# Optimization experiments

Hardware: AMD Instinct MI355X
Metric: run time of the kernel (lower is better)

## Reference

```python
import jax, jax.numpy as jnp
import numpy as np

N, IN, H, OUT, C = 1024, 64, 64, 64, 32
EPS = 1e-5   # SAKELayer.epsilon
INF = 1e5    # SAKELayer.inf


def _w(key, i, o, scale=1.0):
    return jax.random.normal(key, (i, o), jnp.float32) * (scale / np.sqrt(i))


def setup_inputs() -> dict:
    key = jax.random.key(0)
    ks = jax.random.split(key, 16)
    return dict(
        h=jax.random.normal(ks[0], (N, IN), jnp.float32),
        x=jax.random.normal(ks[1], (N, 3), jnp.float32),
        # edge model (ConcatenationFilter): Linear(2*IN+1,H), SiLU, Linear(H,H)
        ew1=_w(ks[2], 2 * IN + 1, H), eb1=jnp.zeros((H,), jnp.float32),
        ew2=_w(ks[3], H, H), eb2=jnp.zeros((H,), jnp.float32),
        # node_mlp: Linear(2H+IN,H), SiLU, Linear(H,OUT)
        nw1=_w(ks[4], 2 * H + IN, H), nb1=jnp.zeros((H,), jnp.float32),
        nw2=_w(ks[5], H, OUT), nb2=jnp.zeros((OUT,), jnp.float32),
        # coordinate_mlp: Linear(H,H), SiLU, Linear(H,1,bias=False) xavier gain 1e-3
        cw1=_w(ks[6], H, H), cb1=jnp.zeros((H,), jnp.float32),
        cw2=_w(ks[7], H, 1, scale=1e-3),
        # semantic_attention_mlp: Linear(H,1), LeakyReLU
        aw=_w(ks[8], H, 1), ab=jnp.zeros((1,), jnp.float32),
        # coefficients_mlp: Linear(H,H), SiLU, Linear(H,C)
        fw1=_w(ks[9], H, H), fb1=jnp.zeros((H,), jnp.float32),
        fw2=_w(ks[10], H, C), fb2=jnp.zeros((C,), jnp.float32),
        # post_norm_mlp: Linear(C,H), SiLU, Linear(H,H)
        pw1=_w(ks[11], C, H), pb1=jnp.zeros((H,), jnp.float32),
        pw2=_w(ks[12], H, H), pb2=jnp.zeros((H,), jnp.float32),
        log_gamma=jnp.array(0.0, jnp.float32),
    )


def reference(h, x, ew1, eb1, ew2, eb2, nw1, nb1, nw2, nb2, cw1, cb1, cw2,
              aw, ab, fw1, fb1, fw2, fb2, pw1, pb1, pw2, pb2, log_gamma):
    n, d_in = h.shape
    silu = jax.nn.silu
    eye = jnp.eye(n, dtype=h.dtype)[:, :, None]                    # [n,n,1]

    x_minus_xt = x[:, None, :] - x[None, :, :]                     # [n,n,3]
    norm = jnp.sqrt(jnp.sum(x_minus_xt ** 2, -1, keepdims=True) + EPS)  # [n,n,1]

    h_cat_ht = jnp.concatenate(
        [jnp.broadcast_to(h[:, None, :], (n, n, d_in)),
         jnp.broadcast_to(h[None, :, :], (n, n, d_in))], -1)       # [n,n,2*IN]

    # edge model: MLP over concat(features, distance)
    e_in = jnp.concatenate([h_cat_ht, norm], -1)                   # [n,n,2*IN+1]
    h_e = silu(e_in @ ew1 + eb1) @ ew2 + eb2                       # [n,n,H]

    # euclidean attention over neighbors j (diag masked by +INF distance)
    att_e = jax.nn.softmax(-(norm + INF * eye) * jnp.exp(log_gamma), axis=1)
    # semantic attention
    att_s = jax.nn.softmax(jax.nn.leaky_relu(h_e @ aw + ab) - INF * eye, axis=1)
    comb = att_e * att_s
    comb = comb / (jnp.sum(comb, axis=1, keepdims=True) + EPS)     # [n,n,1]
    h_e_att = h_e * comb                                           # [n,n,H]

    # spatial attention: equivariant coefficient combinations
    coeff = silu(h_e_att @ fw1 + fb1) @ fw2 + fb2                  # [n,n,C]
    dirs = x_minus_xt / (norm + 1.0)                               # [n,n,3]
    combos = jnp.einsum('ijc,ijd->icd', coeff, dirs) / n           # mean over j -> [n,C,3]
    h_comb = silu(jnp.sum(combos ** 2, -1) @ pw1 + pb1) @ pw2 + pb2  # [n,H]

    # node update
    h_agg = jnp.sum(h_e_att, axis=1)                               # [n,H]
    node_in = jnp.concatenate([h, h_agg, h_comb], -1)              # [n,2H+IN]
    h_out = h + (silu(node_in @ nw1 + nb1) @ nw2 + nb2)            # residual

    # equivariant coordinate update
    phi = silu(h_e @ cw1 + cb1) @ cw2                              # [n,n,1]
    x_out = x + jnp.mean(x_minus_xt * phi, axis=1)                 # [n,3]
    return h_out, x_out
```

## Files before the change

### kernel.cpp

```cpp
#include <hip/hip_runtime.h>
#include <hip/hip_bf16.h>

#define NN 1024
#define JT 128
#define LSTR 72
#define EPSV 1e-5f
#define BIGINF 1e5f

typedef __attribute__((ext_vector_type(8))) short short8;
typedef __attribute__((ext_vector_type(4))) short short4v;
typedef __attribute__((ext_vector_type(4))) float f32x4;

__device__ __forceinline__ float siluf(float v) {
    return v * __builtin_amdgcn_rcpf(1.0f + __expf(-v));
}
__device__ __forceinline__ float pnorm(float dx, float dy, float dz) {
    return sqrtf(dx * dx + dy * dy + dz * dz + EPSV);
}
__device__ __forceinline__ float wsum(float v) {
#pragma unroll
    for (int off = 32; off > 0; off >>= 1) v += __shfl_xor(v, off, 64);
    return v;
}
__device__ __forceinline__ float red16(float v) {
    v += __shfl_xor(v, 1, 64); v += __shfl_xor(v, 2, 64);
    v += __shfl_xor(v, 4, 64); v += __shfl_xor(v, 8, 64);
    return v;
}
__device__ __forceinline__ float redquad(float v) {
    v += __shfl_xor(v, 16, 64); v += __shfl_xor(v, 32, 64);
    return v;
}
__device__ __forceinline__ short f2bs(float v) {
    __hip_bfloat16 b = __float2bfloat16(v);
    return *reinterpret_cast<short*>(&b);
}
__device__ __forceinline__ short f2bt(float v) {
    return (short)(__float_as_uint(v) >> 16);
}

__global__ void kA(const float* __restrict__ h, const float* __restrict__ ew1,
                   const float* __restrict__ eb1, const float* __restrict__ ew2,
                   const float* __restrict__ cw1, const float* __restrict__ fw1,
                   const float* __restrict__ fw2, const float* __restrict__ aw,
                   const float* __restrict__ ab, const float* __restrict__ eb2,
                   float* __restrict__ HA, float* __restrict__ HB,
                   float* __restrict__ HBT, short* __restrict__ ew2T,
                   short* __restrict__ cw1T, short* __restrict__ fw1T,
                   short* __restrict__ fw2T, float* __restrict__ wsv,
                   float* __restrict__ svb) {
    const int b = blockIdx.x;
    const int o = threadIdx.x;
    if (b < NN) {
        const int i = b;
        float hv = h[i * 64 + o];
        float a = 0.f, bb = eb1[o];
#pragma unroll
        for (int k = 0; k < 64; k++) {
            float hk = __shfl(hv, k, 64);
            a += hk * ew1[k * 64 + o];
            bb += hk * ew1[(64 + k) * 64 + o];
        }
        HA[i * 64 + o] = a;
        HB[i * 64 + o] = bb;
        HBT[o * NN + i] = bb;
    } else if (b < NN + 64) {
        const int r = b - NN;
        ew2T[r * 64 + o] = f2bs(ew2[o * 64 + r]);
        cw1T[r * 64 + o] = f2bs(cw1[o * 64 + r]);
        fw1T[r * 64 + o] = f2bs(fw1[o * 64 + r]);
        if (r < 32) fw2T[r * 64 + o] = f2bs(fw2[o * 32 + r]);
    } else {
        float s = 0.f;
#pragma unroll
        for (int q = 0; q < 64; q++) s += ew2[o * 64 + q] * aw[q];
        wsv[o] = s;
        float e = wsum(eb2[o] * aw[o]);
        if (o == 0) svb[0] = e + ab[0];
    }
}

__global__ __launch_bounds__(256) void kBn(
    const float* __restrict__ x, const float* __restrict__ ew1,
    const float* __restrict__ HA, const float* __restrict__ HBT,
    const float* __restrict__ wsv, const float* __restrict__ svb,
    const float* __restrict__ lg, float* __restrict__ ls,
    float* __restrict__ rowm, float* __restrict__ rowd) {
    const int i = blockIdx.x;
    const int t = threadIdx.x;
    const float* HAi = HA + i * 64;
    const float* w1 = ew1 + 128 * 64;
    const float gamma = __expf(lg[0]);
    const float svb0 = svb[0];
    const float xi0 = x[i * 3 + 0], xi1 = x[i * 3 + 1], xi2 = x[i * 3 + 2];

    float4 xa = ((const float4*)x)[3 * t + 0];
    float4 xb = ((const float4*)x)[3 * t + 1];
    float4 xc = ((const float4*)x)[3 * t + 2];
    float nrm[4], le[4], lv[4];
    {
        float dx0 = xi0 - xa.x, dy0 = xi1 - xa.y, dz0 = xi2 - xa.z;
        float dx1 = xi0 - xa.w, dy1 = xi1 - xb.x, dz1 = xi2 - xb.y;
        float dx2 = xi0 - xb.z, dy2 = xi1 - xb.w, dz2 = xi2 - xc.x;
        float dx3 = xi0 - xc.y, dy3 = xi1 - xc.z, dz3 = xi2 - xc.w;
        nrm[0] = pnorm(dx0, dy0, dz0);
        nrm[1] = pnorm(dx1, dy1, dz1);
        nrm[2] = pnorm(dx2, dy2, dz2);
        nrm[3] = pnorm(dx3, dy3, dz3);
    }
    float d0 = 0.f, d1 = 0.f, d2 = 0.f, d3 = 0.f;
#pragma unroll 8
    for (int k = 0; k < 64; k++) {
        float4 hb = *(const float4*)&HBT[k * NN + 4 * t];
        float hk = HAi[k], w1k = w1[k], wv = wsv[k];
        d0 += siluf(hk + hb.x + nrm[0] * w1k) * wv;
        d1 += siluf(hk + hb.y + nrm[1] * w1k) * wv;
        d2 += siluf(hk + hb.z + nrm[2] * w1k) * wv;
        d3 += siluf(hk + hb.w + nrm[3] * w1k) * wv;
    }
    float me = -3.0e38f, ms = -3.0e38f;
    float4 svo;
    {
        float dd[4] = {d0, d1, d2, d3};
#pragma unroll
        for (int m = 0; m < 4; m++) {
            int j = 4 * t + m;
            float sv = dd[m] + svb0;
            sv = sv >= 0.f ? sv : 0.01f * sv;
            if (j == i) sv -= BIGINF;
            lv[m] = sv;
            le[m] = -(nrm[m] + (j == i ? BIGINF : 0.f)) * gamma;
            me = fmaxf(me, le[m]);
            ms = fmaxf(ms, lv[m]);
        }
        svo.x = lv[0]; svo.y = lv[1]; svo.z = lv[2]; svo.w = lv[3];
    }
    *(float4*)&ls[(size_t)i * NN + 4 * t] = svo;

    __shared__ float sm[4], ss[4], s1[4], s2[4], s3[4];
#pragma unroll
    for (int off = 32; off > 0; off >>= 1) {
        me = fmaxf(me, __shfl_xor(me, off, 64));
        ms = fmaxf(ms, __shfl_xor(ms, off, 64));
    }
    const int w = t >> 6;
    if ((t & 63) == 0) { sm[w] = me; ss[w] = ms; }
    __syncthreads();
    me = fmaxf(fmaxf(sm[0], sm[1]), fmaxf(sm[2], sm[3]));
    ms = fmaxf(fmaxf(ss[0], ss[1]), fmaxf(ss[2], ss[3]));
    float Se = 0.f, Ss = 0.f, Sq = 0.f;
#pragma unroll
    for (int m = 0; m < 4; m++) {
        float ee = __expf(le[m] - me);
        float es = __expf(lv[m] - ms);
        Se += ee; Ss += es; Sq += ee * es;
    }
    Se = wsum(Se); Ss = wsum(Ss); Sq = wsum(Sq);
    if ((t & 63) == 0) { s1[w] = Se; s2[w] = Ss; s3[w] = Sq; }
    __syncthreads();
    if (t == 0) {
        rowm[i] = me + ms;
        rowd[i] = (s3[0] + s3[1] + s3[2] + s3[3]) +
                  EPSV * (s1[0] + s1[1] + s1[2] + s1[3]) * (s2[0] + s2[1] + s2[2] + s2[3]);
    }
}

__device__ __forceinline__ void stageW(const short* __restrict__ g, short* s,
                                       int tid, int rows) {
    for (int c = tid; c < rows * 16; c += 512) {
        int r = c >> 4, q = c & 15;
        *(short4v*)&s[r * LSTR + q * 4] = *(const short4v*)&g[r * 64 + q * 4];
    }
}

__global__ __launch_bounds__(512) void kD(
    const float* __restrict__ x, const float* __restrict__ ew1,
    const float* __restrict__ eb2, const float* __restrict__ cb1,
    const float* __restrict__ cw2, const float* __restrict__ fb1,
    const float* __restrict__ fb2, const float* __restrict__ lg,
    const float* __restrict__ HA, const float* __restrict__ HB,
    const short* __restrict__ ew2T, const short* __restrict__ cw1T,
    const short* __restrict__ fw1T, const short* __restrict__ fw2T,
    const float* __restrict__ ls, const float* __restrict__ rowm,
    const float* __restrict__ rowd, float* __restrict__ hagg,
    float* __restrict__ combos, float* __restrict__ xupd) {
    __shared__ __align__(16) short sHe[JT * LSTR];
    __shared__ __align__(16) short sW[64 * LSTR];
    __shared__ float sNrm[JT], sFx[JT], sFy[JT], sFz[JT];
    __shared__ float sDx[JT], sDy[JT], sDz[JT], sPh[JT];
    __shared__ float sComb[JT], sHag[64], sCombos[96];

    const int tid = threadIdx.x;
    const int i = blockIdx.x;
    const int jbase = blockIdx.y * JT;
    const int lane = tid & 63, w = tid >> 6;
    const int col = lane & 15, quad = lane >> 4;
    const int row = w * 16 + col;

    if (tid < JT) {
        int j = jbase + tid;
        float dx = x[i * 3 + 0] - x[j * 3 + 0];
        float dy = x[i * 3 + 1] - x[j * 3 + 1];
        float dz = x[i * 3 + 2] - x[j * 3 + 2];
        float nrm = pnorm(dx, dy, dz);
        float inv1 = __builtin_amdgcn_rcpf(nrm + 1.0f);
        sNrm[tid] = nrm;
        sDx[tid] = dx; sDy[tid] = dy; sDz[tid] = dz;
        sFx[tid] = dx * inv1; sFy[tid] = dy * inv1; sFz[tid] = dz * inv1;
        float gamma = __expf(lg[0]);
        float le = -(nrm + (j == i ? BIGINF : 0.f)) * gamma;
        sComb[tid] = __expf(le + ls[(size_t)i * NN + j] - rowm[i]) / rowd[i];
    } else if (tid < JT + 64) {
        sHag[tid - JT] = 0.f;
    } else if (tid < JT + 160) {
        sCombos[tid - JT - 64] = 0.f;
    }
    stageW(ew2T, sW, tid, 64);
    __syncthreads();

    f32x4 acc[4] = {{0.f, 0.f, 0.f, 0.f}, {0.f, 0.f, 0.f, 0.f},
                    {0.f, 0.f, 0.f, 0.f}, {0.f, 0.f, 0.f, 0.f}};
    {
        const int j = jbase + row;
        const float nrm = sNrm[row];
        short8 afr[2];
#pragma unroll
        for (int kb = 0; kb < 2; kb++) {
            const int k0 = kb * 32 + quad * 8;
            const float* hb = &HB[j * 64 + k0];
            const float* ha = &HA[i * 64 + k0];
            const float* w1 = &ew1[128 * 64 + k0];
#pragma unroll
            for (int t = 0; t < 8; t++)
                afr[kb][t] = f2bt(siluf(ha[t] + hb[t] + nrm * w1[t]));
        }
#pragma unroll
        for (int kb = 0; kb < 2; kb++) {
#pragma unroll
            for (int nb = 0; nb < 4; nb++) {
                short8 b = *(const short8*)&sW[(nb * 16 + col) * LSTR + kb * 32 + quad * 8];
                acc[nb] = __builtin_amdgcn_mfma_f32_16x16x32_bf16(afr[kb], b, acc[nb], 0, 0, 0);
            }
        }
    }
    {
        float eb[4];
#pragma unroll
        for (int nb = 0; nb < 4; nb++) eb[nb] = eb2[nb * 16 + col];
        float hv[4][4];
#pragma unroll
        for (int reg = 0; reg < 4; reg++) {
            int r = w * 16 + quad * 4 + reg;
#pragma unroll
            for (int nb = 0; nb < 4; nb++) {
                hv[nb][reg] = acc[nb][reg] + eb[nb];
                sHe[r * LSTR + nb * 16 + col] = f2bt(hv[nb][reg]);
            }
        }
#pragma unroll
        for (int nb = 0; nb < 4; nb++) {
            float v = 0.f;
#pragma unroll
            for (int reg = 0; reg < 4; reg++)
                v += hv[nb][reg] * sComb[w * 16 + quad * 4 + reg];
            v = redquad(v);
            if (quad == 0) atomicAdd(&sHag[nb * 16 + col], v);
        }
    }
    __syncthreads();
    stageW(cw1T, sW, tid, 64);
    __syncthreads();

    {
        f32x4 p[4] = {{0.f, 0.f, 0.f, 0.f}, {0.f, 0.f, 0.f, 0.f},
                      {0.f, 0.f, 0.f, 0.f}, {0.f, 0.f, 0.f, 0.f}};
        const short* ap = &sHe[row * LSTR + quad * 8];
#pragma unroll
        for (int kb = 0; kb < 2; kb++) {
            short8 a = *(const short8*)&ap[kb * 32];
#pragma unroll
            for (int nb = 0; nb < 4; nb++) {
                short8 b = *(const short8*)&sW[(nb * 16 + col) * LSTR + kb * 32 + quad * 8];
                p[nb] = __builtin_amdgcn_mfma_f32_16x16x32_bf16(a, b, p[nb], 0, 0, 0);
            }
        }
        float cbv[4], cwv[4];
#pragma unroll
        for (int nb = 0; nb < 4; nb++) { cbv[nb] = cb1[nb * 16 + col]; cwv[nb] = cw2[nb * 16 + col]; }
#pragma unroll
        for (int reg = 0; reg < 4; reg++) {
            float ph = 0.f;
#pragma unroll
            for (int nb = 0; nb < 4; nb++) ph += siluf(p[nb][reg] + cbv[nb]) * cwv[nb];
            ph = red16(ph);
            if (col == 0) sPh[w * 16 + quad * 4 + reg] = ph;
        }
    }
    __syncthreads();
    stageW(fw1T, sW, tid, 64);
    __syncthreads();

    f32x4 vacc[4] = {{0.f, 0.f, 0.f, 0.f}, {0.f, 0.f, 0.f, 0.f},
                     {0.f, 0.f, 0.f, 0.f}, {0.f, 0.f, 0.f, 0.f}};
    {
        const short* ap = &sHe[row * LSTR + quad * 8];
#pragma unroll
        for (int kb = 0; kb < 2; kb++) {
            short8 a = *(const short8*)&ap[kb * 32];
#pragma unroll
            for (int nb = 0; nb < 4; nb++) {
                short8 b = *(const short8*)&sW[(nb * 16 + col) * LSTR + kb * 32 + quad * 8];
                vacc[nb] = __builtin_amdgcn_mfma_f32_16x16x32_bf16(a, b, vacc[nb], 0, 0, 0);
            }
        }
    }
    short wvs[4][4];
    {
        float fbv[4];
#pragma unroll
        for (int nb = 0; nb < 4; nb++) fbv[nb] = fb1[nb * 16 + col];
#pragma unroll
        for (int reg = 0; reg < 4; reg++) {
            float cm = sComb[w * 16 + quad * 4 + reg];
#pragma unroll
            for (int nb = 0; nb < 4; nb++)
                wvs[reg][nb] = f2bt(siluf(cm * vacc[nb][reg] + fbv[nb]));
        }
    }
    __syncthreads();
#pragma unroll
    for (int reg = 0; reg < 4; reg++) {
        int r = w * 16 + quad * 4 + reg;
#pragma unroll
        for (int nb = 0; nb < 4; nb++)
            sHe[r * LSTR + nb * 16 + col] = wvs[reg][nb];
    }
    stageW(fw2T, sW, tid, 32);
    __syncthreads();

    {
        f32x4 cacc[2] = {{0.f, 0.f, 0.f, 0.f}, {0.f, 0.f, 0.f, 0.f}};
        const short* ap = &sHe[row * LSTR + quad * 8];
#pragma unroll
        for (int kb = 0; kb < 2; kb++) {
            short8 a = *(const short8*)&ap[kb * 32];
#pragma unroll
            for (int nb = 0; nb < 2; nb++) {
                short8 b = *(const short8*)&sW[(nb * 16 + col) * LSTR + kb * 32 + quad * 8];
                cacc[nb] = __builtin_amdgcn_mfma_f32_16x16x32_bf16(a, b, cacc[nb], 0, 0, 0);
            }
        }
#pragma unroll
        for (int nb = 0; nb < 2; nb++) {
            float fb2v = fb2[nb * 16 + col];
            float px = 0.f, py = 0.f, pz = 0.f;
#pragma unroll
            for (int reg = 0; reg < 4; reg++) {
                int r = w * 16 + quad * 4 + reg;
                float cf = cacc[nb][reg] + fb2v;
                px += cf * sFx[r]; py += cf * sFy[r]; pz += cf * sFz[r];
            }
            px = redquad(px); py = redquad(py); pz = redquad(pz);
            if (quad == 0) {
                int c = nb * 16 + col;
                atomicAdd(&sCombos[c * 3 + 0], px);
                atomicAdd(&sCombos[c * 3 + 1], py);
                atomicAdd(&sCombos[c * 3 + 2], pz);
            }
        }
    }
    __syncthreads();
    if (tid < 64) atomicAdd(&hagg[i * 64 + tid], sHag[tid]);
    if (tid < JT) {
        float xa0 = wsum(sPh[tid] * sDx[tid]);
        float xa1 = wsum(sPh[tid] * sDy[tid]);
        float xa2 = wsum(sPh[tid] * sDz[tid]);
        if ((tid & 63) == 0) {
            atomicAdd(&xupd[i * 3 + 0], xa0);
            atomicAdd(&xupd[i * 3 + 1], xa1);
            atomicAdd(&xupd[i * 3 + 2], xa2);
        }
    }
    if (tid >= JT + 64 && tid < JT + 160) {
        int c = tid - JT - 64;
        atomicAdd(&combos[i * 96 + c], sCombos[c]);
    }
}

__global__ void kE(const float* __restrict__ h, const float* __restrict__ x,
                   const float* __restrict__ nw1, const float* __restrict__ nb1,
                   const float* __restrict__ nw2, const float* __restrict__ nb2,
                   const float* __restrict__ pw1, const float* __restrict__ pb1,
                   const float* __restrict__ pw2, const float* __restrict__ pb2,
                   const float* __restrict__ hagg, const float* __restrict__ combos,
                   const float* __restrict__ xupd, float* __restrict__ out) {
    const int i = blockIdx.x, o = threadIdx.x;
    const float invN = 1.0f / (float)NN;
    float r = 0.f;
    if (o < 32) {
        float v0 = combos[i * 96 + o * 3 + 0] * invN;
        float v1 = combos[i * 96 + o * 3 + 1] * invN;
        float v2 = combos[i * 96 + o * 3 + 2] * invN;
        r = v0 * v0 + v1 * v1 + v2 * v2;
    }
    float t1 = pb1[o];
#pragma unroll
    for (int k = 0; k < 32; k++) t1 += __shfl(r, k, 64) * pw1[k * 64 + o];
    t1 = siluf(t1);
    float hc = pb2[o];
#pragma unroll
    for (int k = 0; k < 64; k++) hc += __shfl(t1, k, 64) * pw2[k * 64 + o];
    float hi = h[i * 64 + o];
    float ha = hagg[i * 64 + o];
    float t2 = nb1[o];
#pragma unroll
    for (int k = 0; k < 64; k++) t2 += __shfl(hi, k, 64) * nw1[k * 64 + o];
#pragma unroll
    for (int k = 0; k < 64; k++) t2 += __shfl(ha, k, 64) * nw1[(64 + k) * 64 + o];
#pragma unroll
    for (int k = 0; k < 64; k++) t2 += __shfl(hc, k, 64) * nw1[(128 + k) * 64 + o];
    t2 = siluf(t2);
    float ho = hi + nb2[o];
#pragma unroll
    for (int k = 0; k < 64; k++) ho += __shfl(t2, k, 64) * nw2[k * 64 + o];
    out[i * 64 + o] = ho;
    if (o < 3)
        out[NN * 64 + i * 3 + o] = x[i * 3 + o] + xupd[i * 3 + o] * invN;
}

extern "C" void kernel_launch(void* const* d_in, const int* in_sizes, int n_in,
                              void* d_out, int out_size, void* d_ws, size_t ws_size,
                              hipStream_t stream) {
    (void)in_sizes; (void)n_in; (void)out_size; (void)ws_size;
    const float* h   = (const float*)d_in[0];
    const float* x   = (const float*)d_in[1];
    const float* ew1 = (const float*)d_in[2];
    const float* eb1 = (const float*)d_in[3];
    const float* ew2 = (const float*)d_in[4];
    const float* eb2 = (const float*)d_in[5];
    const float* nw1 = (const float*)d_in[6];
    const float* nb1 = (const float*)d_in[7];
    const float* nw2 = (const float*)d_in[8];
    const float* nb2 = (const float*)d_in[9];
    const float* cw1 = (const float*)d_in[10];
    const float* cb1 = (const float*)d_in[11];
    const float* cw2 = (const float*)d_in[12];
    const float* aw  = (const float*)d_in[13];
    const float* ab  = (const float*)d_in[14];
    const float* fw1 = (const float*)d_in[15];
    const float* fb1 = (const float*)d_in[16];
    const float* fw2 = (const float*)d_in[17];
    const float* fb2 = (const float*)d_in[18];
    const float* pw1 = (const float*)d_in[19];
    const float* pb1 = (const float*)d_in[20];
    const float* pw2 = (const float*)d_in[21];
    const float* pb2 = (const float*)d_in[22];
    const float* lg  = (const float*)d_in[23];
    float* out = (float*)d_out;

    float* W      = (float*)d_ws;
    float* ls     = W;
    float* HA     = ls + (size_t)NN * NN;
    float* HB     = HA + NN * 64;
    float* HBT    = HB + NN * 64;
    float* rowm   = HBT + NN * 64;
    float* rowd   = rowm + NN;
    float* hagg   = rowd + NN;
    float* combos = hagg + NN * 64;
    float* xupd   = combos + NN * 96;
    float* wsv    = xupd + NN * 3;
    float* svb    = wsv + 64;
    short* ew2T   = (short*)(svb + 4);
    short* cw1T   = ew2T + 64 * 64;
    short* fw1T   = cw1T + 64 * 64;
    short* fw2T   = fw1T + 64 * 64;

    hipMemsetAsync(hagg, 0, (size_t)(NN * 64 + NN * 96 + NN * 3) * sizeof(float), stream);
    kA<<<NN + 65, 64, 0, stream>>>(h, ew1, eb1, ew2, cw1, fw1, fw2, aw, ab, eb2,
                                   HA, HB, HBT, ew2T, cw1T, fw1T, fw2T, wsv, svb);
    kBn<<<NN, 256, 0, stream>>>(x, ew1, HA, HBT, wsv, svb, lg, ls, rowm, rowd);
    dim3 g2(NN, NN / JT);
    kD<<<g2, 512, 0, stream>>>(x, ew1, eb2, cb1, cw2, fb1, fb2, lg, HA, HB,
                               ew2T, cw1T, fw1T, fw2T, ls, rowm, rowd,
                               hagg, combos, xupd);
    kE<<<NN, 64, 0, stream>>>(h, x, nw1, nb1, nw2, nb2, pw1, pb1, pw2, pb2,
                              hagg, combos, xupd, out);
}
```

Before: 303.0 us.

## Stage all edge weights up front and use per-wave scratch to drop block barriers

All four weight matrices are now staged into separate shared buffers once at kernel start, instead of restaging one shared buffer between stages. Each wave keeps its 16-row edge tile in a private scratch buffer. Per-row geometry and attention values live in registers and are broadcast with shuffles, so the intermediate block-wide barriers are removed. This raises shared memory per block, which may lower occupancy, in exchange for fewer synchronisations and shared round trips.

```diff
diff --git a/kernel.cpp b/kernel.cpp
--- a/kernel.cpp
+++ b/kernel.cpp
@@ -184,61 +184,62 @@
     const float* __restrict__ ls, const float* __restrict__ rowm,
     const float* __restrict__ rowd, float* __restrict__ hagg,
     float* __restrict__ combos, float* __restrict__ xupd) {
-    __shared__ __align__(16) short sHe[JT * LSTR];
-    __shared__ __align__(16) short sW[64 * LSTR];
-    __shared__ float sNrm[JT], sFx[JT], sFy[JT], sFz[JT];
-    __shared__ float sDx[JT], sDy[JT], sDz[JT], sPh[JT];
-    __shared__ float sComb[JT], sHag[64], sCombos[96];
+    __shared__ __align__(16) short sWe[64 * LSTR];
+    __shared__ __align__(16) short sWc[64 * LSTR];
+    __shared__ __align__(16) short sWf[64 * LSTR];
+    __shared__ __align__(16) short sW2[32 * LSTR];
+    __shared__ __align__(16) short sScr[8][16 * LSTR];
+    __shared__ float sHag[64], sCombos[96], sXupd[3];
 
     const int tid = threadIdx.x;
     const int i = blockIdx.x;
     const int jbase = blockIdx.y * JT;
     const int lane = tid & 63, w = tid >> 6;
     const int col = lane & 15, quad = lane >> 4;
-    const int row = w * 16 + col;
-
-    if (tid < JT) {
-        int j = jbase + tid;
-        float dx = x[i * 3 + 0] - x[j * 3 + 0];
-        float dy = x[i * 3 + 1] - x[j * 3 + 1];
-        float dz = x[i * 3 + 2] - x[j * 3 + 2];
-        float nrm = pnorm(dx, dy, dz);
-        float inv1 = __builtin_amdgcn_rcpf(nrm + 1.0f);
-        sNrm[tid] = nrm;
-        sDx[tid] = dx; sDy[tid] = dy; sDz[tid] = dz;
-        sFx[tid] = dx * inv1; sFy[tid] = dy * inv1; sFz[tid] = dz * inv1;
+
+    if (tid < 64) sHag[tid] = 0.f;
+    else if (tid < 160) sCombos[tid - 64] = 0.f;
+    else if (tid < 163) sXupd[tid - 160] = 0.f;
+    stageW(ew2T, sWe, tid, 64);
+    stageW(cw1T, sWc, tid, 64);
+    stageW(fw1T, sWf, tid, 64);
+    stageW(fw2T, sW2, tid, 32);
+    __syncthreads();
+
+    short* scr = sScr[w];
+    const int jrow = jbase + w * 16 + col;
+    float dxv, dyv, dzv, nrmv, combv, fxv, fyv, fzv;
+    {
+        dxv = x[i * 3 + 0] - x[jrow * 3 + 0];
+        dyv = x[i * 3 + 1] - x[jrow * 3 + 1];
+        dzv = x[i * 3 + 2] - x[jrow * 3 + 2];
+        nrmv = pnorm(dxv, dyv, dzv);
+        float inv1 = __builtin_amdgcn_rcpf(nrmv + 1.0f);
+        fxv = dxv * inv1; fyv = dyv * inv1; fzv = dzv * inv1;
         float gamma = __expf(lg[0]);
-        float le = -(nrm + (j == i ? BIGINF : 0.f)) * gamma;
-        sComb[tid] = __expf(le + ls[(size_t)i * NN + j] - rowm[i]) / rowd[i];
-    } else if (tid < JT + 64) {
-        sHag[tid - JT] = 0.f;
-    } else if (tid < JT + 160) {
-        sCombos[tid - JT - 64] = 0.f;
-    }
-    stageW(ew2T, sW, tid, 64);
-    __syncthreads();
+        float le = -(nrmv + (jrow == i ? BIGINF : 0.f)) * gamma;
+        combv = __expf(le + ls[(size_t)i * NN + jrow] - rowm[i]) / rowd[i];
+    }
 
     f32x4 acc[4] = {{0.f, 0.f, 0.f, 0.f}, {0.f, 0.f, 0.f, 0.f},
                     {0.f, 0.f, 0.f, 0.f}, {0.f, 0.f, 0.f, 0.f}};
     {
-        const int j = jbase + row;
-        const float nrm = sNrm[row];
         short8 afr[2];
 #pragma unroll
         for (int kb = 0; kb < 2; kb++) {
             const int k0 = kb * 32 + quad * 8;
-            const float* hb = &HB[j * 64 + k0];
+            const float* hb = &HB[jrow * 64 + k0];
             const float* ha = &HA[i * 64 + k0];
             const float* w1 = &ew1[128 * 64 + k0];
 #pragma unroll
             for (int t = 0; t < 8; t++)
-                afr[kb][t] = f2bt(siluf(ha[t] + hb[t] + nrm * w1[t]));
+                afr[kb][t] = f2bt(siluf(ha[t] + hb[t] + nrmv * w1[t]));
         }
 #pragma unroll
         for (int kb = 0; kb < 2; kb++) {
 #pragma unroll
             for (int nb = 0; nb < 4; nb++) {
-                short8 b = *(const short8*)&sW[(nb * 16 + col) * LSTR + kb * 32 + quad * 8];
+                short8 b = *(const short8*)&sWe[(nb * 16 + col) * LSTR + kb * 32 + quad * 8];
                 acc[nb] = __builtin_amdgcn_mfma_f32_16x16x32_bf16(afr[kb], b, acc[nb], 0, 0, 0);
             }
         }
@@ -247,108 +248,96 @@
         float eb[4];
 #pragma unroll
         for (int nb = 0; nb < 4; nb++) eb[nb] = eb2[nb * 16 + col];
-        float hv[4][4];
+        float hv[4][4], cmb[4];
+#pragma unroll
+        for (int reg = 0; reg < 4; reg++) cmb[reg] = __shfl(combv, quad * 4 + reg, 64);
 #pragma unroll
         for (int reg = 0; reg < 4; reg++) {
-            int r = w * 16 + quad * 4 + reg;
 #pragma unroll
             for (int nb = 0; nb < 4; nb++) {
                 hv[nb][reg] = acc[nb][reg] + eb[nb];
-                sHe[r * LSTR + nb * 16 + col] = f2bt(hv[nb][reg]);
+                scr[(quad * 4 + reg) * LSTR + nb * 16 + col] = f2bt(hv[nb][reg]);
             }
         }
 #pragma unroll
         for (int nb = 0; nb < 4; nb++) {
             float v = 0.f;
 #pragma unroll
-            for (int reg = 0; reg < 4; reg++)
-                v += hv[nb][reg] * sComb[w * 16 + quad * 4 + reg];
+            for (int reg = 0; reg < 4; reg++) v += hv[nb][reg] * cmb[reg];
             v = redquad(v);
             if (quad == 0) atomicAdd(&sHag[nb * 16 + col], v);
         }
     }
-    __syncthreads();
-    stageW(cw1T, sW, tid, 64);
-    __syncthreads();
+    short8 a0 = *(const short8*)&scr[col * LSTR + quad * 8];
+    short8 a1 = *(const short8*)&scr[col * LSTR + 32 + quad * 8];
 
     {
         f32x4 p[4] = {{0.f, 0.f, 0.f, 0.f}, {0.f, 0.f, 0.f, 0.f},
                       {0.f, 0.f, 0.f, 0.f}, {0.f, 0.f, 0.f, 0.f}};
-        const short* ap = &sHe[row * LSTR + quad * 8];
-#pragma unroll
-        for (int kb = 0; kb < 2; kb++) {
-            short8 a = *(const short8*)&ap[kb * 32];
-#pragma unroll
-            for (int nb = 0; nb < 4; nb++) {
-                short8 b = *(const short8*)&sW[(nb * 16 + col) * LSTR + kb * 32 + quad * 8];
-                p[nb] = __builtin_amdgcn_mfma_f32_16x16x32_bf16(a, b, p[nb], 0, 0, 0);
-            }
+#pragma unroll
+        for (int nb = 0; nb < 4; nb++) {
+            short8 b0 = *(const short8*)&sWc[(nb * 16 + col) * LSTR + quad * 8];
+            short8 b1 = *(const short8*)&sWc[(nb * 16 + col) * LSTR + 32 + quad * 8];
+            p[nb] = __builtin_amdgcn_mfma_f32_16x16x32_bf16(a0, b0, p[nb], 0, 0, 0);
+            p[nb] = __builtin_amdgcn_mfma_f32_16x16x32_bf16(a1, b1, p[nb], 0, 0, 0);
         }
         float cbv[4], cwv[4];
 #pragma unroll
         for (int nb = 0; nb < 4; nb++) { cbv[nb] = cb1[nb * 16 + col]; cwv[nb] = cw2[nb * 16 + col]; }
+        float xa0 = 0.f, xa1 = 0.f, xa2 = 0.f;
 #pragma unroll
         for (int reg = 0; reg < 4; reg++) {
             float ph = 0.f;
 #pragma unroll
             for (int nb = 0; nb < 4; nb++) ph += siluf(p[nb][reg] + cbv[nb]) * cwv[nb];
             ph = red16(ph);
-            if (col == 0) sPh[w * 16 + quad * 4 + reg] = ph;
-        }
-    }
-    __syncthreads();
-    stageW(fw1T, sW, tid, 64);
-    __syncthreads();
-
-    f32x4 vacc[4] = {{0.f, 0.f, 0.f, 0.f}, {0.f, 0.f, 0.f, 0.f},
-                     {0.f, 0.f, 0.f, 0.f}, {0.f, 0.f, 0.f, 0.f}};
-    {
-        const short* ap = &sHe[row * LSTR + quad * 8];
-#pragma unroll
-        for (int kb = 0; kb < 2; kb++) {
-            short8 a = *(const short8*)&ap[kb * 32];
-#pragma unroll
-            for (int nb = 0; nb < 4; nb++) {
-                short8 b = *(const short8*)&sW[(nb * 16 + col) * LSTR + kb * 32 + quad * 8];
-                vacc[nb] = __builtin_amdgcn_mfma_f32_16x16x32_bf16(a, b, vacc[nb], 0, 0, 0);
-            }
-        }
-    }
-    short wvs[4][4];
-    {
-        float fbv[4];
+            float tdx = __shfl(dxv, quad * 4 + reg, 64);
+            float tdy = __shfl(dyv, quad * 4 + reg, 64);
+            float tdz = __shfl(dzv, quad * 4 + reg, 64);
+            if (col == 0) { xa0 += ph * tdx; xa1 += ph * tdy; xa2 += ph * tdz; }
+        }
+        xa0 = wsum(xa0); xa1 = wsum(xa1); xa2 = wsum(xa2);
+        if (lane == 0) {
+            atomicAdd(&sXupd[0], xa0);
+            atomicAdd(&sXupd[1], xa1);
+            atomicAdd(&sXupd[2], xa2);
+        }
+    }
+
+    {
+        f32x4 vacc[4] = {{0.f, 0.f, 0.f, 0.f}, {0.f, 0.f, 0.f, 0.f},
+                         {0.f, 0.f, 0.f, 0.f}, {0.f, 0.f, 0.f, 0.f}};
+#pragma unroll
+        for (int nb = 0; nb < 4; nb++) {
+            short8 b0 = *(const short8*)&sWf[(nb * 16 + col) * LSTR + quad * 8];
+            short8 b1 = *(const short8*)&sWf[(nb * 16 + col) * LSTR + 32 + quad * 8];
+            vacc[nb] = __builtin_amdgcn_mfma_f32_16x16x32_bf16(a0, b0, vacc[nb], 0, 0, 0);
+            vacc[nb] = __builtin_amdgcn_mfma_f32_16x16x32_bf16(a1, b1, vacc[nb], 0, 0, 0);
+        }
+        float fbv[4], cmb[4];
 #pragma unroll
         for (int nb = 0; nb < 4; nb++) fbv[nb] = fb1[nb * 16 + col];
 #pragma unroll
+        for (int reg = 0; reg < 4; reg++) cmb[reg] = __shfl(combv, quad * 4 + reg, 64);
+#pragma unroll
         for (int reg = 0; reg < 4; reg++) {
-            float cm = sComb[w * 16 + quad * 4 + reg];
 #pragma unroll
             for (int nb = 0; nb < 4; nb++)
-                wvs[reg][nb] = f2bt(siluf(cm * vacc[nb][reg] + fbv[nb]));
-        }
-    }
-    __syncthreads();
-#pragma unroll
-    for (int reg = 0; reg < 4; reg++) {
-        int r = w * 16 + quad * 4 + reg;
-#pragma unroll
-        for (int nb = 0; nb < 4; nb++)
-            sHe[r * LSTR + nb * 16 + col] = wvs[reg][nb];
-    }
-    stageW(fw2T, sW, tid, 32);
-    __syncthreads();
+                scr[(quad * 4 + reg) * LSTR + nb * 16 + col] =
+                    f2bt(siluf(cmb[reg] * vacc[nb][reg] + fbv[nb]));
+        }
+    }
+    short8 wa0 = *(const short8*)&scr[col * LSTR + quad * 8];
+    short8 wa1 = *(const short8*)&scr[col * LSTR + 32 + quad * 8];
 
     {
         f32x4 cacc[2] = {{0.f, 0.f, 0.f, 0.f}, {0.f, 0.f, 0.f, 0.f}};
-        const short* ap = &sHe[row * LSTR + quad * 8];
-#pragma unroll
-        for (int kb = 0; kb < 2; kb++) {
-            short8 a = *(const short8*)&ap[kb * 32];
-#pragma unroll
-            for (int nb = 0; nb < 2; nb++) {
-                short8 b = *(const short8*)&sW[(nb * 16 + col) * LSTR + kb * 32 + quad * 8];
-                cacc[nb] = __builtin_amdgcn_mfma_f32_16x16x32_bf16(a, b, cacc[nb], 0, 0, 0);
-            }
+#pragma unroll
+        for (int nb = 0; nb < 2; nb++) {
+            short8 b0 = *(const short8*)&sW2[(nb * 16 + col) * LSTR + quad * 8];
+            short8 b1 = *(const short8*)&sW2[(nb * 16 + col) * LSTR + 32 + quad * 8];
+            cacc[nb] = __builtin_amdgcn_mfma_f32_16x16x32_bf16(wa0, b0, cacc[nb], 0, 0, 0);
+            cacc[nb] = __builtin_amdgcn_mfma_f32_16x16x32_bf16(wa1, b1, cacc[nb], 0, 0, 0);
         }
 #pragma unroll
         for (int nb = 0; nb < 2; nb++) {
@@ -356,9 +345,11 @@
             float px = 0.f, py = 0.f, pz = 0.f;
 #pragma unroll
             for (int reg = 0; reg < 4; reg++) {
-                int r = w * 16 + quad * 4 + reg;
                 float cf = cacc[nb][reg] + fb2v;
-                px += cf * sFx[r]; py += cf * sFy[r]; pz += cf * sFz[r];
+                float tfx = __shfl(fxv, quad * 4 + reg, 64);
+                float tfy = __shfl(fyv, quad * 4 + reg, 64);
+                float tfz = __shfl(fzv, quad * 4 + reg, 64);
+                px += cf * tfx; py += cf * tfy; pz += cf * tfz;
             }
             px = redquad(px); py = redquad(py); pz = redquad(pz);
             if (quad == 0) {
@@ -371,20 +362,8 @@
     }
     __syncthreads();
     if (tid < 64) atomicAdd(&hagg[i * 64 + tid], sHag[tid]);
-    if (tid < JT) {
-        float xa0 = wsum(sPh[tid] * sDx[tid]);
-        float xa1 = wsum(sPh[tid] * sDy[tid]);
-        float xa2 = wsum(sPh[tid] * sDz[tid]);
-        if ((tid & 63) == 0) {
-            atomicAdd(&xupd[i * 3 + 0], xa0);
-            atomicAdd(&xupd[i * 3 + 1], xa1);
-            atomicAdd(&xupd[i * 3 + 2], xa2);
-        }
-    }
-    if (tid >= JT + 64 && tid < JT + 160) {
-        int c = tid - JT - 64;
-        atomicAdd(&combos[i * 96 + c], sCombos[c]);
-    }
+    else if (tid >= 64 && tid < 160) atomicAdd(&combos[i * 96 + tid - 64], sCombos[tid - 64]);
+    else if (tid >= 160 && tid < 163) atomicAdd(&xupd[i * 3 + tid - 160], sXupd[tid - 160]);
 }
 
 __global__ void kE(const float* __restrict__ h, const float* __restrict__ x,
```

After: 310.6 us. +2.5%, slower.
